# Kernel tuning notes

Measured on AMD Instinct MI355X. Metric: run time of the kernel, lower is better.

Reference implementation:

```python
import jax, jax.numpy as jnp
import numpy as np

G, T, S, M = 128, 512, 24, 4


def setup_inputs() -> dict:
    key = jax.random.key(0)
    k0, k1, k2, k3, k4 = jax.random.split(key, 5)
    inp = jax.random.normal(k0, (G, T, M), dtype=jnp.float32)
    # Stable-ish transition matrices: near 0.95*I
    F = 0.95 * jnp.eye(S, dtype=jnp.float32) + 0.05 * jax.random.normal(k1, (G, T, S, S), dtype=jnp.float32) / jnp.sqrt(S)
    # PSD process noise Q = c*A A^T + eps*I
    Aq = jax.random.normal(k2, (G, T, S, S), dtype=jnp.float32)
    Q = (0.01 / S) * jnp.einsum('gtik,gtjk->gtij', Aq, Aq) + 1e-3 * jnp.eye(S, dtype=jnp.float32)
    H = 0.5 * jax.random.normal(k3, (G, T, M, S), dtype=jnp.float32)
    # PSD measurement noise R
    Ar = jax.random.normal(k4, (G, T, M, M), dtype=jnp.float32)
    R = (0.1 / M) * jnp.einsum('gtik,gtjk->gtij', Ar, Ar) + 1e-2 * jnp.eye(M, dtype=jnp.float32)
    init_mean = jnp.zeros((G, S), dtype=jnp.float32)
    init_cov = jnp.broadcast_to(jnp.eye(S, dtype=jnp.float32), (G, S, S))
    return dict(input=inp, F=F, Q=Q, H=H, R=R, init_mean=init_mean, init_cov=init_cov)


def _measure(m, P, Hc, Rc):
    # one-step-ahead measurement distribution: mu = H m, Sig = H P H^T + R
    mu = jnp.einsum('gms,gs->gm', Hc, m)
    Sig = Hc @ P @ Hc.swapaxes(-1, -2) + Rc
    return mu, Sig


def _kalman(input, F, Q, H, R, init_mean, init_cov):
    # time-major for scan
    y = jnp.moveaxis(input, 1, 0)      # [T,G,M]
    Ft = jnp.moveaxis(F, 1, 0)         # [T,G,S,S]
    Qt = jnp.moveaxis(Q, 1, 0)
    Ht = jnp.moveaxis(H, 1, 0)         # [T,G,M,S]
    Rt = jnp.moveaxis(R, 1, 0)         # [T,G,M,M]

    mu0, Sig0 = _measure(init_mean, init_cov, Ht[0], Rt[0])

    def step(carry, x):
        m, P = carry                     # state prediction for t-1: [G,S], [G,S,S]
        yprev, Fp, Qp, Hp, Rp, Hc, Rc = x
        # --- update with obs at t-1 (using H,R from the t-1 measurement) ---
        HP = Hp @ P                      # [G,M,S]
        Sm = HP @ Hp.swapaxes(-1, -2) + Rp   # innovation cov [G,M,M]
        # K = P H^T S^{-1}; using symmetry: K = solve(S, H P)^T
        K = jnp.linalg.solve(Sm, HP).swapaxes(-1, -2)  # [G,S,M]
        resid = yprev - jnp.einsum('gms,gs->gm', Hp, m)
        m_u = m + jnp.einsum('gsm,gm->gs', K, resid)
        P_u = P - K @ HP
        # --- predict to t ---
        m_p = jnp.einsum('gij,gj->gi', Fp, m_u)
        P_p = Fp @ P_u @ Fp.swapaxes(-1, -2) + Qp
        # --- measurement at t ---
        mu, Sig = _measure(m_p, P_p, Hc, Rc)
        return (m_p, P_p), (mu, Sig)

    xs = (y[:-1], Ft[:-1], Qt[:-1], Ht[:-1], Rt[:-1], Ht[1:], Rt[1:])
    _, (mus, Sigs) = jax.lax.scan(step, (init_mean, init_cov), xs)
    means = jnp.moveaxis(jnp.concatenate([mu0[None], mus], axis=0), 0, 1)   # [G,T,M]
    covs = jnp.moveaxis(jnp.concatenate([Sig0[None], Sigs], axis=0), 0, 1)  # [G,T,M,M]
    return means, covs


def reference(input, F, Q, H, R, init_mean, init_cov):
    return _kalman(input, F, Q, H, R, init_mean, init_cov)
```

## Files before the change

### kernel.cpp

```cpp
#include <hip/hip_runtime.h>

#define Gn 128
#define Tn 512
#define Sn 24
#define SP 28
#define Mn 4
#define COVS_BASE (Gn * Tn * Mn)

__device__ __forceinline__ float4 ld4(const float* p) {
    return *reinterpret_cast<const float4*>(p);
}
__device__ __forceinline__ void st4(float* p, float4 v) {
    *reinterpret_cast<float4*>(p) = v;
}
__device__ __forceinline__ float dot4(float4 a, float4 b) {
    return a.x*b.x + a.y*b.y + a.z*b.z + a.w*b.w;
}

struct Row24 { float4 v[6]; };

__device__ __forceinline__ Row24 loadRow(const float* p) {
    Row24 r;
#pragma unroll
    for (int i = 0; i < 6; ++i) r.v[i] = ld4(p + 4*i);
    return r;
}

__device__ __forceinline__ float dot24(const Row24& a, const float* b) {
    float4 b0 = ld4(b+0), b1 = ld4(b+4), b2 = ld4(b+8),
           b3 = ld4(b+12), b4 = ld4(b+16), b5 = ld4(b+20);
    float s0 = dot4(a.v[0], b0);
    float s1 = dot4(a.v[1], b1);
    float s2 = dot4(a.v[2], b2);
    float s3 = dot4(a.v[3], b3);
    float s4 = dot4(a.v[4], b4);
    float s5 = dot4(a.v[5], b5);
    return ((s0+s1)+(s2+s3))+(s4+s5);
}

__device__ __forceinline__ float dot24rr(const Row24& a, const Row24& b) {
    float s0 = dot4(a.v[0], b.v[0]);
    float s1 = dot4(a.v[1], b.v[1]);
    float s2 = dot4(a.v[2], b.v[2]);
    float s3 = dot4(a.v[3], b.v[3]);
    float s4 = dot4(a.v[4], b.v[4]);
    float s5 = dot4(a.v[5], b.v[5]);
    return ((s0+s1)+(s2+s3))+(s4+s5);
}

__device__ __forceinline__ void barrierLds() {
    asm volatile("s_waitcnt lgkmcnt(0)" ::: "memory");
    __builtin_amdgcn_s_barrier();
    asm volatile("" ::: "memory");
}
__device__ __forceinline__ void waveLds() {
    asm volatile("s_waitcnt lgkmcnt(0)" ::: "memory");
    __builtin_amdgcn_wave_barrier();
    asm volatile("" ::: "memory");
}

extern "C" __global__ void __launch_bounds__(256)
kalman_kernel(const float* __restrict__ y_g, const float* __restrict__ F_g,
              const float* __restrict__ Q_g, const float* __restrict__ H_g,
              const float* __restrict__ R_g, const float* __restrict__ m0_g,
              const float* __restrict__ P0_g, float* __restrict__ out)
{
    const int g   = blockIdx.x;
    const int tid = threadIdx.x;
    const int gT  = g * Tn;

    __shared__ __align__(16) float sP[Sn*SP];
    __shared__ __align__(16) float sFP[Sn*SP];
    __shared__ __align__(16) float sF[2][Sn*SP];
    __shared__ __align__(16) float sQ[2][Sn*SP];
    __shared__ __align__(16) float sH[2][Mn*SP];
    __shared__ __align__(16) float sR[2][16];
    __shared__ __align__(16) float sy[2][4];
    __shared__ __align__(16) float sHP[Mn*SP];
    __shared__ __align__(16) float sW[Sn*4];
    __shared__ __align__(16) float sSig[16];
    __shared__ __align__(16) float sInv[16];
    __shared__ __align__(16) float sMean[Sn];
    __shared__ __align__(16) float sFm[Sn];
    __shared__ __align__(16) float sResid[4];

    const float4* F4 = reinterpret_cast<const float4*>(F_g);
    const float4* Q4 = reinterpret_cast<const float4*>(Q_g);
    const float4* H4 = reinterpret_cast<const float4*>(H_g);
    const float4* R4 = reinterpret_cast<const float4*>(R_g);
    const float4* y4 = reinterpret_cast<const float4*>(y_g);

    auto stage_load = [&](int v, int t) -> float4 {
        if (v < 144)      return F4[(gT + t)*144 + v];
        else if (v < 288) return Q4[(gT + t)*144 + (v-144)];
        else if (v < 312) return H4[(gT + t)*24  + (v-288)];
        else if (v < 316) return R4[(gT + t)*4   + (v-312)];
        else              return y4[gT + t];
    };
    auto stage_store = [&](int v, int bb, float4 val) {
        if (v < 144)      { int r = v/6,        c = (v%6)*4;       st4(&sF[bb][r*SP+c], val); }
        else if (v < 288) { int v2 = v-144; int r = v2/6, c = (v2%6)*4; st4(&sQ[bb][r*SP+c], val); }
        else if (v < 312) { int v2 = v-288; int r = v2/6, c = (v2%6)*4; st4(&sH[bb][r*SP+c], val); }
        else if (v < 316) { st4(&sR[bb][(v-312)*4], val); }
        else              { st4(&sy[bb][0], val); }
    };

    if (tid < 144) {
        int r = tid / 6, c = (tid % 6) * 4;
        st4(&sP[r*SP + c], ld4(&P0_g[g*Sn*Sn + tid*4]));
    } else if (tid < 150) {
        int v = tid - 144;
        st4(&sMean[v*4], ld4(&m0_g[g*Sn + v*4]));
    }
    {
        float4 a0 = stage_load(tid, 0);
        stage_store(tid, 0, a0);
        if (tid + 256 < 317) {
            float4 a1 = stage_load(tid + 256, 0);
            stage_store(tid + 256, 0, a1);
        }
    }
    barrierLds();

    const int w    = tid >> 6;
    const int lane = tid & 63;
    const int ib   = lane >> 3, jb = lane & 7;
    const int i0   = 3*ib, j0 = 3*jb;
    const int a2   = lane / 24,        s2 = lane % 24;
    const int a3   = (64+lane) / 24,   s3 = (64+lane) % 24;
    const int iW   = lane >> 1,        aW = (lane & 1) * 2;

    float4 pf0, pf1;

    for (int t = 0; t < Tn; ++t) {
        const int  b    = t & 1;
        const int  b1   = b ^ 1;
        const bool last = (t == Tn - 1);

        if (!last) {
            pf0 = stage_load(tid, t+1);
            if (tid + 256 < 317) pf1 = stage_load(tid + 256, t+1);
        }

        if (w == 0) {
            if (!last) {
                Row24 p0r = loadRow(&sP[(j0+0)*SP]);
                Row24 p1r = loadRow(&sP[(j0+1)*SP]);
                Row24 p2r = loadRow(&sP[(j0+2)*SP]);
#pragma unroll
                for (int r = 0; r < 3; ++r) {
                    Row24 fr = loadRow(&sF[b][(i0+r)*SP]);
                    sFP[(i0+r)*SP + j0+0] = dot24rr(fr, p0r);
                    sFP[(i0+r)*SP + j0+1] = dot24rr(fr, p1r);
                    sFP[(i0+r)*SP + j0+2] = dot24rr(fr, p2r);
                }
            }
        } else if (w == 1) {
            if (lane < 24 && !last) {
                Row24 fr = loadRow(&sF[b][lane*SP]);
                sFm[lane] = dot24(fr, sMean);
            }
        } else if (w == 2) {
            Row24 hr = loadRow(&sH[b][a2*SP]);
            sHP[a2*SP + s2] = dot24(hr, &sP[s2*SP]);
        } else {
            if (lane < 32) {
                Row24 hr = loadRow(&sH[b][a3*SP]);
                sHP[a3*SP + s3] = dot24(hr, &sP[s3*SP]);
            } else if (lane < 36) {
                int a = lane - 32;
                Row24 hr = loadRow(&sH[b][a*SP]);
                float mu = dot24(hr, sMean);
                out[(gT + t)*4 + a] = mu;
                sResid[a] = sy[b][a] - mu;
            }
        }
        barrierLds();

        float acc[3][3];
        if (w == 1) {
            if (!last) {
                Row24 fr0 = loadRow(&sF[b][(j0+0)*SP]);
                Row24 fr1 = loadRow(&sF[b][(j0+1)*SP]);
                Row24 fr2 = loadRow(&sF[b][(j0+2)*SP]);
#pragma unroll
                for (int r = 0; r < 3; ++r) {
                    Row24 fp = loadRow(&sFP[(i0+r)*SP]);
                    acc[r][0] = dot24rr(fp, fr0);
                    acc[r][1] = dot24rr(fp, fr1);
                    acc[r][2] = dot24rr(fp, fr2);
                }
            }
        } else if (w == 2) {
            if (lane < 48 && !last) {
                Row24 fp = loadRow(&sFP[iW*SP]);
                sW[iW*4 + aW]     = dot24(fp, &sH[b][aW*SP]);
                sW[iW*4 + aW + 1] = dot24(fp, &sH[b][(aW+1)*SP]);
            }
        } else if (w == 3) {
            if (lane < 16) {
                int a = lane >> 2, bb = lane & 3;
                Row24 hp = loadRow(&sHP[a*SP]);
                float sig = dot24(hp, &sH[b][bb*SP]) + sR[b][lane];
                sSig[lane] = sig;
                out[COVS_BASE + (size_t)(gT + t)*16 + lane] = sig;
            }
            if (!last) {
                waveLds();
                if (lane < 16) {
                    float s00=sSig[0],  s01=sSig[1],  s02=sSig[2],  s03=sSig[3];
                    float s10=sSig[4],  s11=sSig[5],  s12=sSig[6],  s13=sSig[7];
                    float s20=sSig[8],  s21=sSig[9],  s22=sSig[10], s23=sSig[11];
                    float s30=sSig[12], s31=sSig[13], s32=sSig[14], s33=sSig[15];
                    float p0 = s00*s11 - s01*s10;
                    float p1 = s00*s12 - s02*s10;
                    float p2 = s00*s13 - s03*s10;
                    float p3 = s01*s12 - s02*s11;
                    float p4 = s01*s13 - s03*s11;
                    float p5 = s02*s13 - s03*s12;
                    float q0c = s20*s31 - s21*s30;
                    float q1c = s20*s32 - s22*s30;
                    float q2c = s20*s33 - s23*s30;
                    float q3c = s21*s32 - s22*s31;
                    float q4c = s21*s33 - s23*s31;
                    float q5c = s22*s33 - s23*s32;
                    float det  = p0*q5c - p1*q4c + p2*q3c + p3*q2c - p4*q1c + p5*q0c;
                    float rdet = 1.0f / det;
                    int ia = lane >> 2, ic = lane & 3;
                    int r0 = (ic==0)?1:0, r1 = (ic<=1)?2:1, r2 = (ic<=2)?3:2;
                    int u0 = (ia==0)?1:0, u1 = (ia<=1)?2:1, u2 = (ia<=2)?3:2;
                    float m00=sSig[r0*4+u0], m01=sSig[r0*4+u1], m02=sSig[r0*4+u2];
                    float m10=sSig[r1*4+u0], m11=sSig[r1*4+u1], m12=sSig[r1*4+u2];
                    float m20=sSig[r2*4+u0], m21=sSig[r2*4+u1], m22=sSig[r2*4+u2];
                    float minor = m00*(m11*m22 - m12*m21)
                                - m01*(m10*m22 - m12*m20)
                                + m02*(m10*m21 - m11*m20);
                    float cof = ((ia + ic) & 1) ? -minor : minor;
                    sInv[lane] = cof * rdet;
                }
            }
        }
        if (last) return;
        barrierLds();

        if (w == 1) {
            float4 inv0 = ld4(&sInv[0]),  inv1 = ld4(&sInv[4]);
            float4 inv2 = ld4(&sInv[8]),  inv3 = ld4(&sInv[12]);
            float4 wj0 = ld4(&sW[(j0+0)*4]);
            float4 wj1 = ld4(&sW[(j0+1)*4]);
            float4 wj2 = ld4(&sW[(j0+2)*4]);
#pragma unroll
            for (int r = 0; r < 3; ++r) {
                float4 wi = ld4(&sW[(i0+r)*4]);
                float4 X  = make_float4(dot4(wi,inv0), dot4(wi,inv1),
                                        dot4(wi,inv2), dot4(wi,inv3));
                sP[(i0+r)*SP + j0+0] = acc[r][0] + sQ[b][(i0+r)*SP + j0+0] - dot4(X, wj0);
                sP[(i0+r)*SP + j0+1] = acc[r][1] + sQ[b][(i0+r)*SP + j0+1] - dot4(X, wj1);
                sP[(i0+r)*SP + j0+2] = acc[r][2] + sQ[b][(i0+r)*SP + j0+2] - dot4(X, wj2);
            }
        } else if (w == 2) {
            if (lane < 24) {
                float4 inv0 = ld4(&sInv[0]),  inv1 = ld4(&sInv[4]);
                float4 inv2 = ld4(&sInv[8]),  inv3 = ld4(&sInv[12]);
                float4 ws = ld4(&sW[lane*4]);
                float4 Xs = make_float4(dot4(ws,inv0), dot4(ws,inv1),
                                        dot4(ws,inv2), dot4(ws,inv3));
                sMean[lane] = sFm[lane] + dot4(Xs, ld4(&sResid[0]));
            }
        }
        stage_store(tid, b1, pf0);
        if (tid + 256 < 317) stage_store(tid + 256, b1, pf1);
        barrierLds();
    }
}

extern "C" void kernel_launch(void* const* d_in, const int* in_sizes, int n_in,
                              void* d_out, int out_size, void* d_ws, size_t ws_size,
                              hipStream_t stream) {
    kalman_kernel<<<Gn, 256, 0, stream>>>(
        (const float*)d_in[0], (const float*)d_in[1], (const float*)d_in[2],
        (const float*)d_in[3], (const float*)d_in[4], (const float*)d_in[5],
        (const float*)d_in[6], (float*)d_out);
}
```

Baseline: 1.316 ms.

## Collapse Kalman step to a single wavefront with readlane broadcasts

Each filter now runs on one 64-lane wavefront instead of four warps. All block-wide barriers become wave-local waits, and the 4x4 innovation inverse is computed redundantly in every lane from readlane-broadcast values, so the sSig/sInv LDS round trips go away. Q is read directly from global memory into registers rather than staged through LDS. The trade-off is that each lane does more serial work per step (both the FP and FPF products) with less parallelism per group, and register pressure goes up.

```diff
diff --git a/kernel.cpp b/kernel.cpp
--- a/kernel.cpp
+++ b/kernel.cpp
@@ -48,89 +48,79 @@
     return ((s0+s1)+(s2+s3))+(s4+s5);
 }
 
-__device__ __forceinline__ void barrierLds() {
-    asm volatile("s_waitcnt lgkmcnt(0)" ::: "memory");
-    __builtin_amdgcn_s_barrier();
-    asm volatile("" ::: "memory");
-}
+__device__ __forceinline__ float rlane(float v, int l) {
+    return __int_as_float(__builtin_amdgcn_readlane(__float_as_int(v), l));
+}
+
 __device__ __forceinline__ void waveLds() {
     asm volatile("s_waitcnt lgkmcnt(0)" ::: "memory");
     __builtin_amdgcn_wave_barrier();
     asm volatile("" ::: "memory");
 }
 
-extern "C" __global__ void __launch_bounds__(256)
+extern "C" __global__ void __launch_bounds__(64, 1)
 kalman_kernel(const float* __restrict__ y_g, const float* __restrict__ F_g,
               const float* __restrict__ Q_g, const float* __restrict__ H_g,
               const float* __restrict__ R_g, const float* __restrict__ m0_g,
               const float* __restrict__ P0_g, float* __restrict__ out)
 {
-    const int g   = blockIdx.x;
-    const int tid = threadIdx.x;
-    const int gT  = g * Tn;
-
-    __shared__ __align__(16) float sP[Sn*SP];
+    const int g    = blockIdx.x;
+    const int lane = threadIdx.x;
+    const int gT   = g * Tn;
+
+    __shared__ __align__(16) float sP [Sn*SP];
     __shared__ __align__(16) float sFP[Sn*SP];
-    __shared__ __align__(16) float sF[2][Sn*SP];
-    __shared__ __align__(16) float sQ[2][Sn*SP];
-    __shared__ __align__(16) float sH[2][Mn*SP];
-    __shared__ __align__(16) float sR[2][16];
-    __shared__ __align__(16) float sy[2][4];
+    __shared__ __align__(16) float sF [2][Sn*SP];
+    __shared__ __align__(16) float sH [2][Mn*SP];
+    __shared__ __align__(16) float sR [2][16];
+    __shared__ __align__(16) float sy [2][4];
     __shared__ __align__(16) float sHP[Mn*SP];
-    __shared__ __align__(16) float sW[Sn*4];
-    __shared__ __align__(16) float sSig[16];
-    __shared__ __align__(16) float sInv[16];
+    __shared__ __align__(16) float sW [Sn*4];
     __shared__ __align__(16) float sMean[Sn];
-    __shared__ __align__(16) float sFm[Sn];
-    __shared__ __align__(16) float sResid[4];
+    __shared__ __align__(16) float sFm [Sn];
 
     const float4* F4 = reinterpret_cast<const float4*>(F_g);
-    const float4* Q4 = reinterpret_cast<const float4*>(Q_g);
     const float4* H4 = reinterpret_cast<const float4*>(H_g);
     const float4* R4 = reinterpret_cast<const float4*>(R_g);
     const float4* y4 = reinterpret_cast<const float4*>(y_g);
 
     auto stage_load = [&](int v, int t) -> float4 {
-        if (v < 144)      return F4[(gT + t)*144 + v];
-        else if (v < 288) return Q4[(gT + t)*144 + (v-144)];
-        else if (v < 312) return H4[(gT + t)*24  + (v-288)];
-        else if (v < 316) return R4[(gT + t)*4   + (v-312)];
+        if (v < 144)      return F4[(size_t)(gT + t)*144 + v];
+        else if (v < 168) return H4[(size_t)(gT + t)*24  + (v-144)];
+        else if (v < 172) return R4[(size_t)(gT + t)*4   + (v-168)];
         else              return y4[gT + t];
     };
     auto stage_store = [&](int v, int bb, float4 val) {
-        if (v < 144)      { int r = v/6,        c = (v%6)*4;       st4(&sF[bb][r*SP+c], val); }
-        else if (v < 288) { int v2 = v-144; int r = v2/6, c = (v2%6)*4; st4(&sQ[bb][r*SP+c], val); }
-        else if (v < 312) { int v2 = v-288; int r = v2/6, c = (v2%6)*4; st4(&sH[bb][r*SP+c], val); }
-        else if (v < 316) { st4(&sR[bb][(v-312)*4], val); }
+        if (v < 144)      { int r = v/6, c = (v%6)*4;               st4(&sF[bb][r*SP+c], val); }
+        else if (v < 168) { int v2 = v-144; int r = v2/6, c = (v2%6)*4; st4(&sH[bb][r*SP+c], val); }
+        else if (v < 172) { st4(&sR[bb][(v-168)*4], val); }
         else              { st4(&sy[bb][0], val); }
     };
 
-    if (tid < 144) {
-        int r = tid / 6, c = (tid % 6) * 4;
-        st4(&sP[r*SP + c], ld4(&P0_g[g*Sn*Sn + tid*4]));
-    } else if (tid < 150) {
-        int v = tid - 144;
-        st4(&sMean[v*4], ld4(&m0_g[g*Sn + v*4]));
+    {
+        int v0 = lane, v1 = lane + 64, v2 = lane + 128;
+        st4(&sP[(v0/6)*SP + (v0%6)*4], ld4(&P0_g[(size_t)g*Sn*Sn + v0*4]));
+        st4(&sP[(v1/6)*SP + (v1%6)*4], ld4(&P0_g[(size_t)g*Sn*Sn + v1*4]));
+        if (lane < 16)
+            st4(&sP[(v2/6)*SP + (v2%6)*4], ld4(&P0_g[(size_t)g*Sn*Sn + v2*4]));
+        if (lane < 6)
+            st4(&sMean[lane*4], ld4(&m0_g[(size_t)g*Sn + lane*4]));
+        stage_store(lane,      0, stage_load(lane,      0));
+        stage_store(lane + 64, 0, stage_load(lane + 64, 0));
+        if (lane < 45) stage_store(lane + 128, 0, stage_load(lane + 128, 0));
     }
-    {
-        float4 a0 = stage_load(tid, 0);
-        stage_store(tid, 0, a0);
-        if (tid + 256 < 317) {
-            float4 a1 = stage_load(tid + 256, 0);
-            stage_store(tid + 256, 0, a1);
-        }
-    }
-    barrierLds();
-
-    const int w    = tid >> 6;
-    const int lane = tid & 63;
-    const int ib   = lane >> 3, jb = lane & 7;
-    const int i0   = 3*ib, j0 = 3*jb;
-    const int a2   = lane / 24,        s2 = lane % 24;
-    const int a3   = (64+lane) / 24,   s3 = (64+lane) % 24;
-    const int iW   = lane >> 1,        aW = (lane & 1) * 2;
-
-    float4 pf0, pf1;
+    waveLds();
+
+    const int ib = lane >> 3, jb = lane & 7;
+    const int i0 = 3*ib, j0 = 3*jb;
+    const int aH = lane / 24, sH_ = lane % 24;
+    const int o2 = 64 + lane;
+    const int aH2 = o2 / 24, sH2 = o2 % 24;
+    const int iW = lane >> 1, aW = (lane & 1)*2;
+    const bool muLane = (lane==1) | (lane==25) | (lane==49);
+    const bool needMean = (jb == 0) | muLane | (lane == 9);
+
+    float4 pf0, pf1, pf2;
 
     for (int t = 0; t < Tn; ++t) {
         const int  b    = t & 1;
@@ -138,146 +128,170 @@
         const bool last = (t == Tn - 1);
 
         if (!last) {
-            pf0 = stage_load(tid, t+1);
-            if (tid + 256 < 317) pf1 = stage_load(tid + 256, t+1);
-        }
-
-        if (w == 0) {
-            if (!last) {
-                Row24 p0r = loadRow(&sP[(j0+0)*SP]);
-                Row24 p1r = loadRow(&sP[(j0+1)*SP]);
-                Row24 p2r = loadRow(&sP[(j0+2)*SP]);
-#pragma unroll
-                for (int r = 0; r < 3; ++r) {
-                    Row24 fr = loadRow(&sF[b][(i0+r)*SP]);
-                    sFP[(i0+r)*SP + j0+0] = dot24rr(fr, p0r);
-                    sFP[(i0+r)*SP + j0+1] = dot24rr(fr, p1r);
-                    sFP[(i0+r)*SP + j0+2] = dot24rr(fr, p2r);
-                }
-            }
-        } else if (w == 1) {
-            if (lane < 24 && !last) {
-                Row24 fr = loadRow(&sF[b][lane*SP]);
-                sFm[lane] = dot24(fr, sMean);
-            }
-        } else if (w == 2) {
-            Row24 hr = loadRow(&sH[b][a2*SP]);
-            sHP[a2*SP + s2] = dot24(hr, &sP[s2*SP]);
-        } else {
-            if (lane < 32) {
-                Row24 hr = loadRow(&sH[b][a3*SP]);
-                sHP[a3*SP + s3] = dot24(hr, &sP[s3*SP]);
-            } else if (lane < 36) {
-                int a = lane - 32;
-                Row24 hr = loadRow(&sH[b][a*SP]);
-                float mu = dot24(hr, sMean);
-                out[(gT + t)*4 + a] = mu;
-                sResid[a] = sy[b][a] - mu;
-            }
-        }
-        barrierLds();
+            pf0 = stage_load(lane,      t+1);
+            pf1 = stage_load(lane + 64, t+1);
+            if (lane < 45) pf2 = stage_load(lane + 128, t+1);
+        }
+        float qv[3][3];
+        if (!last) {
+            const float* Qp = Q_g + (size_t)(gT + t) * 576;
+#pragma unroll
+            for (int r = 0; r < 3; ++r)
+#pragma unroll
+                for (int c = 0; c < 3; ++c)
+                    qv[r][c] = Qp[(i0+r)*24 + j0 + c];
+        }
+
+        Row24 Fi0, Fi1, Fi2;
+        float fp[3][3];
+        if (!last) {
+            Fi0 = loadRow(&sF[b][(i0+0)*SP]);
+            Fi1 = loadRow(&sF[b][(i0+1)*SP]);
+            Fi2 = loadRow(&sF[b][(i0+2)*SP]);
+            Row24 Pj0 = loadRow(&sP[(j0+0)*SP]);
+            Row24 Pj1 = loadRow(&sP[(j0+1)*SP]);
+            Row24 Pj2 = loadRow(&sP[(j0+2)*SP]);
+            fp[0][0] = dot24rr(Fi0, Pj0); fp[0][1] = dot24rr(Fi0, Pj1); fp[0][2] = dot24rr(Fi0, Pj2);
+            fp[1][0] = dot24rr(Fi1, Pj0); fp[1][1] = dot24rr(Fi1, Pj1); fp[1][2] = dot24rr(Fi1, Pj2);
+            fp[2][0] = dot24rr(Fi2, Pj0); fp[2][1] = dot24rr(Fi2, Pj1); fp[2][2] = dot24rr(Fi2, Pj2);
+        }
+        Row24 h1 = loadRow(&sH[b][aH*SP]);
+        float hp1 = dot24(h1, &sP[sH_*SP]);
+        Row24 h2; float hp2 = 0.f;
+        if (lane < 32) {
+            h2 = loadRow(&sH[b][aH2*SP]);
+            hp2 = dot24(h2, &sP[sH2*SP]);
+        }
+        Row24 mr;
+        if (needMean) mr = loadRow(&sMean[0]);
+        float fmv0, fmv1, fmv2;
+        if (jb == 0 && !last) {
+            fmv0 = dot24rr(Fi0, mr);
+            fmv1 = dot24rr(Fi1, mr);
+            fmv2 = dot24rr(Fi2, mr);
+        }
+        float residv = 0.f;
+        if (muLane) {
+            float mu = dot24rr(h1, mr);
+            out[(size_t)(gT + t)*4 + aH] = mu;
+            residv = sy[b][aH] - mu;
+        } else if (lane == 9) {
+            float mu = dot24rr(h2, mr);
+            out[(size_t)(gT + t)*4 + 3] = mu;
+            residv = sy[b][3] - mu;
+        }
+        if (!last) {
+#pragma unroll
+            for (int r = 0; r < 3; ++r)
+#pragma unroll
+                for (int c = 0; c < 3; ++c)
+                    sFP[(i0+r)*SP + j0 + c] = fp[r][c];
+            if (jb == 0) { sFm[i0+0] = fmv0; sFm[i0+1] = fmv1; sFm[i0+2] = fmv2; }
+        }
+        sHP[aH*SP + sH_] = hp1;
+        if (lane < 32) sHP[aH2*SP + sH2] = hp2;
+        waveLds();
+
+        float sigv = 0.f;
+        if (lane >= 48) {
+            int q = lane - 48;
+            int a = q >> 2, c = q & 3;
+            Row24 hpr = loadRow(&sHP[a*SP]);
+            sigv = dot24(hpr, &sH[b][c*SP]) + sR[b][q];
+            out[COVS_BASE + (size_t)(gT + t)*16 + q] = sigv;
+        }
+        if (last) return;
 
         float acc[3][3];
-        if (w == 1) {
-            if (!last) {
-                Row24 fr0 = loadRow(&sF[b][(j0+0)*SP]);
-                Row24 fr1 = loadRow(&sF[b][(j0+1)*SP]);
-                Row24 fr2 = loadRow(&sF[b][(j0+2)*SP]);
-#pragma unroll
-                for (int r = 0; r < 3; ++r) {
-                    Row24 fp = loadRow(&sFP[(i0+r)*SP]);
-                    acc[r][0] = dot24rr(fp, fr0);
-                    acc[r][1] = dot24rr(fp, fr1);
-                    acc[r][2] = dot24rr(fp, fr2);
-                }
-            }
-        } else if (w == 2) {
-            if (lane < 48 && !last) {
-                Row24 fp = loadRow(&sFP[iW*SP]);
-                sW[iW*4 + aW]     = dot24(fp, &sH[b][aW*SP]);
-                sW[iW*4 + aW + 1] = dot24(fp, &sH[b][(aW+1)*SP]);
-            }
-        } else if (w == 3) {
-            if (lane < 16) {
-                int a = lane >> 2, bb = lane & 3;
-                Row24 hp = loadRow(&sHP[a*SP]);
-                float sig = dot24(hp, &sH[b][bb*SP]) + sR[b][lane];
-                sSig[lane] = sig;
-                out[COVS_BASE + (size_t)(gT + t)*16 + lane] = sig;
-            }
-            if (!last) {
-                waveLds();
-                if (lane < 16) {
-                    float s00=sSig[0],  s01=sSig[1],  s02=sSig[2],  s03=sSig[3];
-                    float s10=sSig[4],  s11=sSig[5],  s12=sSig[6],  s13=sSig[7];
-                    float s20=sSig[8],  s21=sSig[9],  s22=sSig[10], s23=sSig[11];
-                    float s30=sSig[12], s31=sSig[13], s32=sSig[14], s33=sSig[15];
-                    float p0 = s00*s11 - s01*s10;
-                    float p1 = s00*s12 - s02*s10;
-                    float p2 = s00*s13 - s03*s10;
-                    float p3 = s01*s12 - s02*s11;
-                    float p4 = s01*s13 - s03*s11;
-                    float p5 = s02*s13 - s03*s12;
-                    float q0c = s20*s31 - s21*s30;
-                    float q1c = s20*s32 - s22*s30;
-                    float q2c = s20*s33 - s23*s30;
-                    float q3c = s21*s32 - s22*s31;
-                    float q4c = s21*s33 - s23*s31;
-                    float q5c = s22*s33 - s23*s32;
-                    float det  = p0*q5c - p1*q4c + p2*q3c + p3*q2c - p4*q1c + p5*q0c;
-                    float rdet = 1.0f / det;
-                    int ia = lane >> 2, ic = lane & 3;
-                    int r0 = (ic==0)?1:0, r1 = (ic<=1)?2:1, r2 = (ic<=2)?3:2;
-                    int u0 = (ia==0)?1:0, u1 = (ia<=1)?2:1, u2 = (ia<=2)?3:2;
-                    float m00=sSig[r0*4+u0], m01=sSig[r0*4+u1], m02=sSig[r0*4+u2];
-                    float m10=sSig[r1*4+u0], m11=sSig[r1*4+u1], m12=sSig[r1*4+u2];
-                    float m20=sSig[r2*4+u0], m21=sSig[r2*4+u1], m22=sSig[r2*4+u2];
-                    float minor = m00*(m11*m22 - m12*m21)
-                                - m01*(m10*m22 - m12*m20)
-                                + m02*(m10*m21 - m11*m20);
-                    float cof = ((ia + ic) & 1) ? -minor : minor;
-                    sInv[lane] = cof * rdet;
-                }
-            }
-        }
-        if (last) return;
-        barrierLds();
-
-        if (w == 1) {
-            float4 inv0 = ld4(&sInv[0]),  inv1 = ld4(&sInv[4]);
-            float4 inv2 = ld4(&sInv[8]),  inv3 = ld4(&sInv[12]);
+        {
+            Row24 FPi0 = loadRow(&sFP[(i0+0)*SP]);
+            Row24 FPi1 = loadRow(&sFP[(i0+1)*SP]);
+            Row24 FPi2 = loadRow(&sFP[(i0+2)*SP]);
+            Row24 Fj0  = loadRow(&sF[b][(j0+0)*SP]);
+            Row24 Fj1  = loadRow(&sF[b][(j0+1)*SP]);
+            Row24 Fj2  = loadRow(&sF[b][(j0+2)*SP]);
+            acc[0][0] = dot24rr(FPi0, Fj0); acc[0][1] = dot24rr(FPi0, Fj1); acc[0][2] = dot24rr(FPi0, Fj2);
+            acc[1][0] = dot24rr(FPi1, Fj0); acc[1][1] = dot24rr(FPi1, Fj1); acc[1][2] = dot24rr(FPi1, Fj2);
+            acc[2][0] = dot24rr(FPi2, Fj0); acc[2][1] = dot24rr(FPi2, Fj1); acc[2][2] = dot24rr(FPi2, Fj2);
+        }
+        if (lane < 48) {
+            Row24 fpw = loadRow(&sFP[iW*SP]);
+            sW[iW*4 + aW]     = dot24(fpw, &sH[b][aW*SP]);
+            sW[iW*4 + aW + 1] = dot24(fpw, &sH[b][(aW+1)*SP]);
+        }
+        float s00 = rlane(sigv,48), s01 = rlane(sigv,49), s02 = rlane(sigv,50), s03 = rlane(sigv,51);
+        float s10 = rlane(sigv,52), s11 = rlane(sigv,53), s12 = rlane(sigv,54), s13 = rlane(sigv,55);
+        float s20 = rlane(sigv,56), s21 = rlane(sigv,57), s22 = rlane(sigv,58), s23 = rlane(sigv,59);
+        float s30 = rlane(sigv,60), s31 = rlane(sigv,61), s32 = rlane(sigv,62), s33 = rlane(sigv,63);
+        float p0 = s00*s11 - s01*s10;
+        float p1 = s00*s12 - s02*s10;
+        float p2 = s00*s13 - s03*s10;
+        float p3 = s01*s12 - s02*s11;
+        float p4 = s01*s13 - s03*s11;
+        float p5 = s02*s13 - s03*s12;
+        float q0 = s20*s31 - s21*s30;
+        float q1 = s20*s32 - s22*s30;
+        float q2 = s20*s33 - s23*s30;
+        float q3 = s21*s32 - s22*s31;
+        float q4 = s21*s33 - s23*s31;
+        float q5 = s22*s33 - s23*s32;
+        float det = p0*q5 - p1*q4 + p2*q3 + p3*q2 - p4*q1 + p5*q0;
+        float rd  = 1.0f / det;
+        float4 invr0 = make_float4(( s11*q5 - s12*q4 + s13*q3)*rd,
+                                   (-s01*q5 + s02*q4 - s03*q3)*rd,
+                                   ( s31*p5 - s32*p4 + s33*p3)*rd,
+                                   (-s21*p5 + s22*p4 - s23*p3)*rd);
+        float4 invr1 = make_float4((-s10*q5 + s12*q2 - s13*q1)*rd,
+                                   ( s00*q5 - s02*q2 + s03*q1)*rd,
+                                   (-s30*p5 + s32*p2 - s33*p1)*rd,
+                                   ( s20*p5 - s22*p2 + s23*p1)*rd);
+        float4 invr2 = make_float4(( s10*q4 - s11*q2 + s13*q0)*rd,
+                                   (-s00*q4 + s01*q2 - s03*q0)*rd,
+                                   ( s30*p4 - s31*p2 + s33*p0)*rd,
+                                   (-s20*p4 + s21*p2 - s23*p0)*rd);
+        float4 invr3 = make_float4((-s10*q3 + s11*q1 - s12*q0)*rd,
+                                   ( s00*q3 - s01*q1 + s02*q0)*rd,
+                                   (-s30*p3 + s31*p1 - s32*p0)*rd,
+                                   ( s20*p3 - s21*p1 + s22*p0)*rd);
+        waveLds();
+
+        {
+            float4 wi0 = ld4(&sW[(i0+0)*4]);
+            float4 wi1 = ld4(&sW[(i0+1)*4]);
+            float4 wi2 = ld4(&sW[(i0+2)*4]);
             float4 wj0 = ld4(&sW[(j0+0)*4]);
             float4 wj1 = ld4(&sW[(j0+1)*4]);
             float4 wj2 = ld4(&sW[(j0+2)*4]);
-#pragma unroll
-            for (int r = 0; r < 3; ++r) {
-                float4 wi = ld4(&sW[(i0+r)*4]);
-                float4 X  = make_float4(dot4(wi,inv0), dot4(wi,inv1),
-                                        dot4(wi,inv2), dot4(wi,inv3));
-                sP[(i0+r)*SP + j0+0] = acc[r][0] + sQ[b][(i0+r)*SP + j0+0] - dot4(X, wj0);
-                sP[(i0+r)*SP + j0+1] = acc[r][1] + sQ[b][(i0+r)*SP + j0+1] - dot4(X, wj1);
-                sP[(i0+r)*SP + j0+2] = acc[r][2] + sQ[b][(i0+r)*SP + j0+2] - dot4(X, wj2);
-            }
-        } else if (w == 2) {
-            if (lane < 24) {
-                float4 inv0 = ld4(&sInv[0]),  inv1 = ld4(&sInv[4]);
-                float4 inv2 = ld4(&sInv[8]),  inv3 = ld4(&sInv[12]);
-                float4 ws = ld4(&sW[lane*4]);
-                float4 Xs = make_float4(dot4(ws,inv0), dot4(ws,inv1),
-                                        dot4(ws,inv2), dot4(ws,inv3));
-                sMean[lane] = sFm[lane] + dot4(Xs, ld4(&sResid[0]));
-            }
-        }
-        stage_store(tid, b1, pf0);
-        if (tid + 256 < 317) stage_store(tid + 256, b1, pf1);
-        barrierLds();
+            float4 X0 = make_float4(dot4(wi0,invr0), dot4(wi0,invr1), dot4(wi0,invr2), dot4(wi0,invr3));
+            float4 X1 = make_float4(dot4(wi1,invr0), dot4(wi1,invr1), dot4(wi1,invr2), dot4(wi1,invr3));
+            float4 X2 = make_float4(dot4(wi2,invr0), dot4(wi2,invr1), dot4(wi2,invr2), dot4(wi2,invr3));
+            sP[(i0+0)*SP + j0+0] = acc[0][0] + qv[0][0] - dot4(X0, wj0);
+            sP[(i0+0)*SP + j0+1] = acc[0][1] + qv[0][1] - dot4(X0, wj1);
+            sP[(i0+0)*SP + j0+2] = acc[0][2] + qv[0][2] - dot4(X0, wj2);
+            sP[(i0+1)*SP + j0+0] = acc[1][0] + qv[1][0] - dot4(X1, wj0);
+            sP[(i0+1)*SP + j0+1] = acc[1][1] + qv[1][1] - dot4(X1, wj1);
+            sP[(i0+1)*SP + j0+2] = acc[1][2] + qv[1][2] - dot4(X1, wj2);
+            sP[(i0+2)*SP + j0+0] = acc[2][0] + qv[2][0] - dot4(X2, wj0);
+            sP[(i0+2)*SP + j0+1] = acc[2][1] + qv[2][1] - dot4(X2, wj1);
+            sP[(i0+2)*SP + j0+2] = acc[2][2] + qv[2][2] - dot4(X2, wj2);
+        }
+        if (lane < 24) {
+            float4 ws = ld4(&sW[lane*4]);
+            float4 Xs = make_float4(dot4(ws,invr0), dot4(ws,invr1), dot4(ws,invr2), dot4(ws,invr3));
+            float4 rs = make_float4(rlane(residv,1), rlane(residv,25), rlane(residv,49), rlane(residv,9));
+            sMean[lane] = sFm[lane] + dot4(Xs, rs);
+        }
+        stage_store(lane,      b1, pf0);
+        stage_store(lane + 64, b1, pf1);
+        if (lane < 45) stage_store(lane + 128, b1, pf2);
+        waveLds();
     }
 }
 
 extern "C" void kernel_launch(void* const* d_in, const int* in_sizes, int n_in,
                               void* d_out, int out_size, void* d_ws, size_t ws_size,
                               hipStream_t stream) {
-    kalman_kernel<<<Gn, 256, 0, stream>>>(
+    kalman_kernel<<<Gn, 64, 0, stream>>>(
         (const float*)d_in[0], (const float*)d_in[1], (const float*)d_in[2],
         (const float*)d_in[3], (const float*)d_in[4], (const float*)d_in[5],
         (const float*)d_in[6], (float*)d_out);
```

After: 2.316 ms. 1.76x slower.
